# Kernel tuning notes

Hardware: AMD Instinct MI355X
Metric: run time of the kernel (lower is better)

## Reference

```python
import jax, jax.numpy as jnp
import numpy as np

EPS = 1e-4          # self.epsilon
STENCIL = 24        # fixed neighbor count


def _apply_G(x, coeffs, neighbors, N):
    """SpMV: y_i = G_ii * x_i + sum_j G_ij * x_{nbr[i,j]}.
    x: [B,N,1], coeffs: [B,N,25], neighbors: [B,N,24] (>=N means invalid)."""
    B = x.shape[0]
    mask = neighbors < N                                   # [B,N,24]
    safe = jnp.where(mask, neighbors, 0)
    x2 = x[..., 0]                                         # [B,N]
    x_nbrs = jnp.take_along_axis(x2, safe.reshape(B, -1), axis=1)
    x_nbrs = x_nbrs.reshape(B, -1, STENCIL) * mask.astype(x.dtype)
    res = x2 * coeffs[:, :, 0] + (x_nbrs * coeffs[:, :, 1:]).sum(axis=2)
    return res[..., None]                                  # [B,N,1]


def _apply_GT(x, coeffs, neighbors, N):
    """Transpose SpMV (scatter-add): y_{nbr[i,j]} += G_ij * x_i."""
    B = x.shape[0]
    mask = neighbors < N
    tgt = jnp.where(mask, neighbors, 0)                    # safe targets; masked vals are 0
    vals = (x * coeffs[:, :, 1:]) * mask.astype(x.dtype)   # [B,N,24]
    res = x[..., 0] * coeffs[:, :, 0]                      # [B,N]
    res = jax.vmap(lambda r, t, v: r.at[t].add(v))(
        res, tgt.reshape(B, -1), vals.reshape(B, -1))
    return res[..., None]                                  # [B,N,1]


def setup_inputs() -> dict:
    key = jax.random.key(0)
    kG, kAd, kAo, kw, kn = jax.random.split(key, 5)
    B, N = 2, 262144
    G_coeffs = jax.random.normal(kG, (B, N, 25), dtype=jnp.float32)
    A_diag = jax.random.normal(kAd, (B, N, 1), dtype=jnp.float32)
    A_off = jax.random.normal(kAo, (B, N, STENCIL), dtype=jnp.float32)
    w = jax.random.normal(kw, (B, N, 1), dtype=jnp.float32)
    valid_mask = jnp.ones((B, N, 1), dtype=jnp.float32)
    neighbors = jax.random.randint(kn, (B, N, STENCIL), 0, 270000, dtype=jnp.int64)
    return {"G_coeffs": G_coeffs, "A_diag": A_diag, "A_off": A_off,
            "w": w, "valid_mask": valid_mask, "neighbors": neighbors}


def reference(G_coeffs, A_diag, A_off, w, valid_mask, neighbors):
    B, N, _ = G_coeffs.shape
    active = valid_mask.sum()
    norm_A = (jnp.abs(A_diag).sum() + jnp.abs(A_off).sum()) / (active * 25 + 1e-6)
    # single probe vector (num_probe_vectors = 1)
    wm = w * valid_mask                                    # probe, masked
    u = _apply_GT(wm, G_coeffs, neighbors, N)
    v = _apply_G(u, G_coeffs, neighbors, N) + EPS * wm
    A_coeffs = jnp.concatenate([A_diag, A_off], axis=2)    # [B,N,25]
    y = _apply_G(v, A_coeffs, neighbors, N)
    z = y / (norm_A + 1e-8)
    diff = (z - wm) * valid_mask
    return (diff ** 2).sum() / (valid_mask.sum() + 1e-6)
```

## Files before the change

kernel.cpp:

```cpp
#include <hip/hip_runtime.h>
#include <stdint.h>

#define STENCIL 24
#define EPS_F 1e-4f
#define BLK 256
#define NXCD 8

#define NODE_N 262144
#define BIN_NODES 2048
#define LBINS 128
#define NBINS 256
#define BIN_CAP_G 49152

#define S_THREADS 512
#define S_EPT 8
#define EDGES_PER_BLOCK (S_THREADS * S_EPT)

typedef int   i32x2 __attribute__((ext_vector_type(2)));
typedef float f32x4 __attribute__((ext_vector_type(4)));

template <typename T>
static __device__ __forceinline__ T ntload(const T* p) {
    return __builtin_nontemporal_load(p);
}

static __device__ __forceinline__ int get_xcc_id() {
    int x;
    asm volatile("s_getreg_b32 %0, hwreg(HW_REG_XCC_ID)" : "=s"(x));
    return x & (NXCD - 1);
}

__device__ __forceinline__ float wave_reduce_f32(float v) {
    #pragma unroll
    for (int off = 32; off > 0; off >>= 1)
        v += __shfl_down(v, off, 64);
    return v;
}

__device__ __forceinline__ void block_reduce5(float v[5], float out[5]) {
    __shared__ float sw[4][5];
    #pragma unroll
    for (int c = 0; c < 5; ++c) v[c] = wave_reduce_f32(v[c]);
    if ((threadIdx.x & 63) == 0) {
        #pragma unroll
        for (int c = 0; c < 5; ++c) sw[threadIdx.x >> 6][c] = v[c];
    }
    __syncthreads();
    if (threadIdx.x == 0) {
        #pragma unroll
        for (int c = 0; c < 5; ++c)
            out[c] = sw[0][c] + sw[1][c] + sw[2][c] + sw[3][c];
    }
}

__global__ __launch_bounds__(S_THREADS)
void k_sortscatter(const float* __restrict__ G, const float* __restrict__ w,
                   const float* __restrict__ mask, const int* __restrict__ nbr,
                   float* __restrict__ u, int* __restrict__ binCnt,
                   int2* __restrict__ pairs) {
    __shared__ int2 rec[EDGES_PER_BLOCK];
    __shared__ int hist[LBINS], incl[LBINS], excl[LBINS], pos[LBINS], gb[LBINS];
    int tid = threadIdx.x;
    if (tid < LBINS) hist[tid] = 0;
    __syncthreads();

    long long blockStart = (long long)blockIdx.x * EDGES_PER_BLOCK;
    long long t0 = blockStart + (long long)tid * S_EPT;

    int nb[S_EPT];
    const int4* p4 = (const int4*)(nbr + t0);
    #pragma unroll
    for (int q = 0; q < S_EPT / 4; ++q) {
        int4 x = p4[q];
        nb[q*4] = x.x; nb[q*4+1] = x.y; nb[q*4+2] = x.z; nb[q*4+3] = x.w;
    }
    #pragma unroll
    for (int e = 0; e < S_EPT; ++e) {
        unsigned n = (unsigned)nb[e];
        if (n < (unsigned)NODE_N) atomicAdd(&hist[n >> 11], 1);
    }
    __syncthreads();

    if (tid < LBINS) incl[tid] = hist[tid];
    __syncthreads();
    for (int d = 1; d < LBINS; d <<= 1) {
        int x = 0;
        if (tid < LBINS && tid >= d) x = incl[tid - d];
        __syncthreads();
        if (tid < LBINS) incl[tid] += x;
        __syncthreads();
    }
    int batchBase = (blockStart >= (long long)NODE_N * STENCIL) ? LBINS : 0;
    if (tid < LBINS) {
        int h = hist[tid];
        int ex = incl[tid] - h;
        excl[tid] = ex;
        pos[tid]  = ex;
        gb[tid]   = h ? atomicAdd(&binCnt[batchBase + tid], h) : 0;
    }
    __syncthreads();

    long long i = t0 / STENCIL;
    int j0 = (int)(t0 - i * STENCIL);
    float wm = w[i] * mask[i];
    if (j0 == 0) u[i] = wm * G[i * 25];
    float gv[S_EPT];
    const float* grow = G + i * 25 + 1 + j0;
    #pragma unroll
    for (int e = 0; e < S_EPT; ++e) gv[e] = grow[e];
    #pragma unroll
    for (int e = 0; e < S_EPT; ++e) {
        unsigned n = (unsigned)nb[e];
        if (n < (unsigned)NODE_N) {
            int b = (int)(n >> 11);
            int lp = atomicAdd(&pos[b], 1);
            rec[lp] = make_int2((int)(n & (BIN_NODES - 1)) | (b << 11),
                                __float_as_int(wm * gv[e]));
        }
    }
    __syncthreads();

    int tot = incl[LBINS - 1];
    for (int s = tid; s < tot; s += S_THREADS) {
        int2 r = rec[s];
        int b = (r.x >> 11) & (LBINS - 1);
        int dst = gb[b] + (s - excl[b]);
        if (dst < BIN_CAP_G)
            pairs[(long long)(batchBase + b) * BIN_CAP_G + dst] =
                make_int2(r.x & (BIN_NODES - 1), r.y);
    }
}

__global__ __launch_bounds__(1024)
void k_binaccum(const int* __restrict__ binCnt, const int2* __restrict__ pairs,
                float* __restrict__ u) {
    __shared__ float acc[4][BIN_NODES + 1];
    int g = blockIdx.x, tid = threadIdx.x;
    for (int l = tid; l < BIN_NODES; l += 1024) {
        acc[0][l] = 0.f; acc[1][l] = 0.f; acc[2][l] = 0.f; acc[3][l] = 0.f;
    }
    __syncthreads();
    int cnt = binCnt[g]; if (cnt > BIN_CAP_G) cnt = BIN_CAP_G;
    const i32x2* pb = (const i32x2*)(pairs + (long long)g * BIN_CAP_G);
    int rep = tid & 3;
    for (int s = tid; s < cnt; s += 1024) {
        i32x2 r = __builtin_nontemporal_load(pb + s);
        atomicAdd(&acc[rep][r.x], __int_as_float(r.y));
    }
    __syncthreads();
    long long gbase = (long long)(g >> 7) * NODE_N + (long long)(g & (LBINS - 1)) * BIN_NODES;
    for (int l = tid; l < BIN_NODES; l += 1024)
        u[gbase + l] += acc[0][l] + acc[1][l] + acc[2][l] + acc[3][l];
}

__global__ __launch_bounds__(BLK)
void k_v(const float* __restrict__ G, const float* __restrict__ w,
         const float* __restrict__ mask, const int* __restrict__ nbr,
         const float* __restrict__ u, float* __restrict__ v, long long BN) {
    __shared__ float sg[BLK * 25];
    int tid = threadIdx.x;
    long long base = (long long)blockIdx.x * BLK;
    int rows = (int)(((BN - base) < BLK) ? (BN - base) : BLK);
    const float* gsrc = G + base * 25;
    for (int k = tid; k < rows * 25; k += BLK) sg[k] = ntload(gsrc + k);
    __syncthreads();
    if (tid >= rows) return;
    long long i = base + tid;
    const int4* nb4 = (const int4*)(nbr + i * STENCIL);
    int nn[24];
    #pragma unroll
    for (int q = 0; q < 6; ++q) {
        int4 x = nb4[q];
        nn[q*4] = x.x; nn[q*4+1] = x.y; nn[q*4+2] = x.z; nn[q*4+3] = x.w;
    }
    const float* g  = sg + tid * 25;
    const float* ub = u + (i / NODE_N) * (long long)NODE_N;
    float uv[STENCIL];
    #pragma unroll
    for (int j = 0; j < STENCIL; ++j)
        uv[j] = ub[(unsigned)nn[j] & (unsigned)(NODE_N - 1)];
    float acc = u[i] * g[0] + EPS_F * ntload(w + i) * ntload(mask + i);
    #pragma unroll
    for (int j = 0; j < STENCIL; ++j)
        acc += g[1 + j] * (((unsigned)nn[j] < (unsigned)NODE_N) ? uv[j] : 0.f);
    v[i] = acc;
}

__global__ __launch_bounds__(BLK)
void k_y2(const float* __restrict__ Ad, const float* __restrict__ Ao,
          const float* __restrict__ w, const float* __restrict__ mask,
          const int* __restrict__ nbr, const float* __restrict__ v,
          float* __restrict__ py, int nblk) {
    int tid = threadIdx.x;
    long long i0 = (long long)blockIdx.x * BLK + tid;
    long long i1 = i0 + NODE_N;
    int nn0[24], nn1[24];
    const int4* nb40 = (const int4*)(nbr + i0 * STENCIL);
    const int4* nb41 = (const int4*)(nbr + i1 * STENCIL);
    #pragma unroll
    for (int q = 0; q < 6; ++q) {
        int4 x = nb40[q];
        nn0[q*4] = x.x; nn0[q*4+1] = x.y; nn0[q*4+2] = x.z; nn0[q*4+3] = x.w;
    }
    #pragma unroll
    for (int q = 0; q < 6; ++q) {
        int4 x = nb41[q];
        nn1[q*4] = x.x; nn1[q*4+1] = x.y; nn1[q*4+2] = x.z; nn1[q*4+3] = x.w;
    }
    const float* vb0 = v;
    const float* vb1 = v + NODE_N;
    float vv0[24], vv1[24];
    unsigned valid0 = 0, valid1 = 0;
    #pragma unroll
    for (int j = 0; j < 24; ++j) {
        vv0[j] = vb0[(unsigned)nn0[j] & (unsigned)(NODE_N - 1)];
        valid0 |= ((unsigned)nn0[j] < (unsigned)NODE_N) ? (1u << j) : 0u;
    }
    #pragma unroll
    for (int j = 0; j < 24; ++j) {
        vv1[j] = vb1[(unsigned)nn1[j] & (unsigned)(NODE_N - 1)];
        valid1 |= ((unsigned)nn1[j] < (unsigned)NODE_N) ? (1u << j) : 0u;
    }
    float a0[24], a1[24];
    const f32x4* ar0 = (const f32x4*)(Ao + i0 * STENCIL);
    const f32x4* ar1 = (const f32x4*)(Ao + i1 * STENCIL);
    #pragma unroll
    for (int q = 0; q < 6; ++q) {
        f32x4 x = ntload(ar0 + q);
        a0[q*4] = x.x; a0[q*4+1] = x.y; a0[q*4+2] = x.z; a0[q*4+3] = x.w;
    }
    #pragma unroll
    for (int q = 0; q < 6; ++q) {
        f32x4 x = ntload(ar1 + q);
        a1[q*4] = x.x; a1[q*4+1] = x.y; a1[q*4+2] = x.z; a1[q*4+3] = x.w;
    }
    float ad0 = ntload(Ad + i0),  ad1 = ntload(Ad + i1);
    float m0  = ntload(mask + i0), m1 = ntload(mask + i1);
    float w0  = ntload(w + i0),    w1 = ntload(w + i1);
    float vi0 = v[i0], vi1 = v[i1];
    float asum = fabsf(ad0) + fabsf(ad1);
    #pragma unroll
    for (int j = 0; j < 24; ++j) asum += fabsf(a0[j]) + fabsf(a1[j]);
    float acc0 = vi0 * ad0, acc1 = vi1 * ad1;
    #pragma unroll
    for (int j = 0; j < 24; ++j) {
        acc0 += a0[j] * (((valid0 >> j) & 1u) ? vv0[j] : 0.f);
        acc1 += a1[j] * (((valid1 >> j) & 1u) ? vv1[j] : 0.f);
    }
    float P0 = acc0 * m0, P1 = acc1 * m1;
    float Q0 = w0 * m0 * m0, Q1 = w1 * m1 * m1;
    float part[5] = {asum, m0 + m1, P0*P0 + P1*P1, P0*Q0 + P1*Q1, Q0*Q0 + Q1*Q1};
    float out[5];
    block_reduce5(part, out);
    if (tid == 0) {
        #pragma unroll
        for (int c = 0; c < 5; ++c) py[(long long)c * nblk + blockIdx.x] = out[c];
    }
}

__global__ __launch_bounds__(BLK)
void k_y(const float* __restrict__ Ad, const float* __restrict__ Ao,
         const float* __restrict__ w, const float* __restrict__ mask,
         const int* __restrict__ nbr, const float* __restrict__ v,
         float* __restrict__ py, int nblk, long long BN) {
    int tid = threadIdx.x;
    long long base = (long long)blockIdx.x * BLK;
    int rows = (int)(((BN - base) < BLK) ? (BN - base) : BLK);
    float part[5] = {0.f, 0.f, 0.f, 0.f, 0.f};
    if (tid < rows) {
        long long i = base + tid;
        const int4* nb4 = (const int4*)(nbr + i * STENCIL);
        int nn[24];
        #pragma unroll
        for (int q = 0; q < 6; ++q) {
            int4 x = nb4[q];
            nn[q*4] = x.x; nn[q*4+1] = x.y; nn[q*4+2] = x.z; nn[q*4+3] = x.w;
        }
        const float* vb = v + (i / NODE_N) * (long long)NODE_N;
        float vv[STENCIL];
        #pragma unroll
        for (int j = 0; j < STENCIL; ++j)
            vv[j] = vb[(unsigned)nn[j] & (unsigned)(NODE_N - 1)];
        float a[STENCIL];
        const f32x4* ar = (const f32x4*)(Ao + i * STENCIL);
        #pragma unroll
        for (int q = 0; q < 6; ++q) {
            f32x4 x = ntload(ar + q);
            a[q*4] = x.x; a[q*4+1] = x.y; a[q*4+2] = x.z; a[q*4+3] = x.w;
        }
        float ad = ntload(Ad + i);
        float m  = ntload(mask + i);
        float wv = ntload(w + i);
        float asum = fabsf(ad);
        #pragma unroll
        for (int j = 0; j < STENCIL; ++j) asum += fabsf(a[j]);
        float acc = v[i] * ad;
        #pragma unroll
        for (int j = 0; j < STENCIL; ++j)
            acc += a[j] * (((unsigned)nn[j] < (unsigned)NODE_N) ? vv[j] : 0.f);
        float P = acc * m;
        float Q = wv * m * m;
        part[0] = asum;
        part[1] = m;
        part[2] = P * P;
        part[3] = P * Q;
        part[4] = Q * Q;
    }
    float out[5];
    block_reduce5(part, out);
    if (tid == 0) {
        #pragma unroll
        for (int c = 0; c < 5; ++c) py[(long long)c * nblk + blockIdx.x] = out[c];
    }
}

__global__ __launch_bounds__(1024)
void k_final(const float* __restrict__ py, int nblk, float* __restrict__ out) {
    __shared__ float sw[16][5];
    __shared__ float res[5];
    float part[5] = {0.f, 0.f, 0.f, 0.f, 0.f};
    for (int t = threadIdx.x; t < nblk; t += 1024) {
        #pragma unroll
        for (int c = 0; c < 5; ++c) part[c] += py[(long long)c * nblk + t];
    }
    #pragma unroll
    for (int c = 0; c < 5; ++c) part[c] = wave_reduce_f32(part[c]);
    if ((threadIdx.x & 63) == 0) {
        #pragma unroll
        for (int c = 0; c < 5; ++c) sw[threadIdx.x >> 6][c] = part[c];
    }
    __syncthreads();
    if (threadIdx.x == 0) {
        #pragma unroll
        for (int c = 0; c < 5; ++c) {
            float r = 0.f;
            for (int k = 0; k < 16; ++k) r += sw[k][c];
            res[c] = r;
        }
        double A   = res[0], act = res[1];
        double a   = res[2], b   = res[3], c2 = res[4];
        double nrm = A / (act * 25.0 + 1e-6) + 1e-8;
        double loss = (a / (nrm * nrm) - 2.0 * b / nrm + c2) / (act + 1e-6);
        out[0] = (float)loss;
    }
}

__global__ void k_init_fb(const float* __restrict__ G, const float* __restrict__ w,
                          const float* __restrict__ mask, float* __restrict__ u, long long BN) {
    long long i = (long long)blockIdx.x * blockDim.x + threadIdx.x;
    if (i < BN) u[i] = w[i] * mask[i] * G[i * 25];
}
__global__ void k_scatter_fb(const float* __restrict__ G, const float* __restrict__ w,
                             const float* __restrict__ mask, const int* __restrict__ nbr,
                             float* __restrict__ ucopy, int N, long long BN) {
    long long t = (long long)blockIdx.x * blockDim.x + threadIdx.x;
    if (t >= BN * STENCIL) return;
    long long i = t / STENCIL;
    int j = (int)(t - i * STENCIL);
    int n = nbr[t];
    if ((unsigned)n >= (unsigned)N) return;
    float wm = w[i] * mask[i];
    float gv = G[i * 25 + 1 + j];
    float* ub = ucopy + (long long)get_xcc_id() * BN + (i / N) * (long long)N;
    __hip_atomic_fetch_add(&ub[n], wm * gv, __ATOMIC_RELAXED, __HIP_MEMORY_SCOPE_WORKGROUP);
}
__global__ void k_usum_fb(const float* __restrict__ ucopy, float* __restrict__ u, long long BN) {
    long long i = (long long)blockIdx.x * blockDim.x + threadIdx.x;
    if (i >= BN) return;
    float acc = u[i];
    #pragma unroll
    for (int c = 0; c < NXCD; ++c) acc += ucopy[(long long)c * BN + i];
    u[i] = acc;
}

extern "C" void kernel_launch(void* const* d_in, const int* in_sizes, int n_in,
                              void* d_out, int out_size, void* d_ws, size_t ws_size,
                              hipStream_t stream) {
    const float* G    = (const float*)d_in[0];
    const float* Ad   = (const float*)d_in[1];
    const float* Ao   = (const float*)d_in[2];
    const float* w    = (const float*)d_in[3];
    const float* mask = (const float*)d_in[4];
    const int*   nbr  = (const int*)d_in[5];

    const long long BN = in_sizes[3];
    const long long nEdges = BN * STENCIL;
    const int nodeBlocks = (int)((BN + BLK - 1) / BLK);

    float* u  = (float*)d_ws;
    float* v  = u + BN;
    float* py = v + BN;
    char*  after_common = (char*)(py + 5LL * nodeBlocks);

    int*  binCnt = (int*)(((uintptr_t)after_common + 15) & ~(uintptr_t)15);
    int2* pairs  = (int2*)(((uintptr_t)(binCnt + NBINS) + 7) & ~(uintptr_t)7);
    size_t need_fast = (size_t)((char*)(pairs + (long long)NBINS * BIN_CAP_G) - (char*)d_ws);

    float* ucopy = (float*)(((uintptr_t)after_common + 15) & ~(uintptr_t)15);

    bool fast = (BN == 2LL * NODE_N) && (nEdges % EDGES_PER_BLOCK == 0) &&
                (ws_size >= need_fast);

    if (fast) {
        hipMemsetAsync(binCnt, 0, NBINS * sizeof(int), stream);
        int gridS = (int)(nEdges / EDGES_PER_BLOCK);
        k_sortscatter<<<gridS, S_THREADS, 0, stream>>>(G, w, mask, nbr, u, binCnt, pairs);
        k_binaccum<<<NBINS, 1024, 0, stream>>>(binCnt, pairs, u);
        k_v<<<nodeBlocks, BLK, 0, stream>>>(G, w, mask, nbr, u, v, BN);
        int yBlocks = NODE_N / BLK;
        k_y2<<<yBlocks, BLK, 0, stream>>>(Ad, Ao, w, mask, nbr, v, py, yBlocks);
        k_final<<<1, 1024, 0, stream>>>(py, yBlocks, (float*)d_out);
    } else {
        hipMemsetAsync(ucopy, 0, (size_t)NXCD * BN * sizeof(float), stream);
        int edgeBlocks = (int)((nEdges + BLK - 1) / BLK);
        k_init_fb<<<nodeBlocks, BLK, 0, stream>>>(G, w, mask, u, BN);
        k_scatter_fb<<<edgeBlocks, BLK, 0, stream>>>(G, w, mask, nbr, ucopy, NODE_N, BN);
        k_usum_fb<<<nodeBlocks, BLK, 0, stream>>>(ucopy, u, BN);
        k_v<<<nodeBlocks, BLK, 0, stream>>>(G, w, mask, nbr, u, v, BN);
        k_y<<<nodeBlocks, BLK, 0, stream>>>(Ad, Ao, w, mask, nbr, v, py, nodeBlocks, BN);
        k_final<<<1, 1024, 0, stream>>>(py, nodeBlocks, (float*)d_out);
    }
}
```

Before: 400.4 us.

## Replace binned pair buffer and accumulation pass with direct sorted global atomics

The transpose scatter no longer writes locally sorted (index, value) pairs to a global binned buffer for a second kernel to accumulate in shared memory. Each block now issues float atomicAdds straight into u in the bin-sorted order, and u is zeroed by a memset while the diagonal term is also added atomically. This drops one kernel launch and the write and re-read of the pairs buffer, at the cost of many global atomics whose per-block locality is only partial. It also removes the capacity clamp that silently dropped overflowing edges.

Measured after the change: 816.1 us. 104% more time.

```diff
diff --git a/kernel.cpp b/kernel.cpp
--- a/kernel.cpp
+++ b/kernel.cpp
@@ -9,8 +9,6 @@
 #define NODE_N 262144
 #define BIN_NODES 2048
 #define LBINS 128
-#define NBINS 256
-#define BIN_CAP_G 49152
 
 #define S_THREADS 512
 #define S_EPT 8
@@ -56,10 +54,9 @@
 __global__ __launch_bounds__(S_THREADS)
 void k_sortscatter(const float* __restrict__ G, const float* __restrict__ w,
                    const float* __restrict__ mask, const int* __restrict__ nbr,
-                   float* __restrict__ u, int* __restrict__ binCnt,
-                   int2* __restrict__ pairs) {
+                   float* __restrict__ u) {
     __shared__ int2 rec[EDGES_PER_BLOCK];
-    __shared__ int hist[LBINS], incl[LBINS], excl[LBINS], pos[LBINS], gb[LBINS];
+    __shared__ int hist[LBINS], incl[LBINS], pos[LBINS];
     int tid = threadIdx.x;
     if (tid < LBINS) hist[tid] = 0;
     __syncthreads();
@@ -90,20 +87,13 @@
         if (tid < LBINS) incl[tid] += x;
         __syncthreads();
     }
-    int batchBase = (blockStart >= (long long)NODE_N * STENCIL) ? LBINS : 0;
-    if (tid < LBINS) {
-        int h = hist[tid];
-        int ex = incl[tid] - h;
-        excl[tid] = ex;
-        pos[tid]  = ex;
-        gb[tid]   = h ? atomicAdd(&binCnt[batchBase + tid], h) : 0;
-    }
+    if (tid < LBINS) pos[tid] = incl[tid] - hist[tid];
     __syncthreads();
 
     long long i = t0 / STENCIL;
     int j0 = (int)(t0 - i * STENCIL);
     float wm = w[i] * mask[i];
-    if (j0 == 0) u[i] = wm * G[i * 25];
+    if (j0 == 0) atomicAdd(&u[i], wm * G[i * 25]);
     float gv[S_EPT];
     const float* grow = G + i * 25 + 1 + j0;
     #pragma unroll
@@ -120,37 +110,14 @@
     }
     __syncthreads();
 
+    long long ubase = (blockStart >= (long long)NODE_N * STENCIL) ? NODE_N : 0;
     int tot = incl[LBINS - 1];
     for (int s = tid; s < tot; s += S_THREADS) {
         int2 r = rec[s];
-        int b = (r.x >> 11) & (LBINS - 1);
-        int dst = gb[b] + (s - excl[b]);
-        if (dst < BIN_CAP_G)
-            pairs[(long long)(batchBase + b) * BIN_CAP_G + dst] =
-                make_int2(r.x & (BIN_NODES - 1), r.y);
-    }
-}
-
-__global__ __launch_bounds__(1024)
-void k_binaccum(const int* __restrict__ binCnt, const int2* __restrict__ pairs,
-                float* __restrict__ u) {
-    __shared__ float acc[4][BIN_NODES + 1];
-    int g = blockIdx.x, tid = threadIdx.x;
-    for (int l = tid; l < BIN_NODES; l += 1024) {
-        acc[0][l] = 0.f; acc[1][l] = 0.f; acc[2][l] = 0.f; acc[3][l] = 0.f;
-    }
-    __syncthreads();
-    int cnt = binCnt[g]; if (cnt > BIN_CAP_G) cnt = BIN_CAP_G;
-    const i32x2* pb = (const i32x2*)(pairs + (long long)g * BIN_CAP_G);
-    int rep = tid & 3;
-    for (int s = tid; s < cnt; s += 1024) {
-        i32x2 r = __builtin_nontemporal_load(pb + s);
-        atomicAdd(&acc[rep][r.x], __int_as_float(r.y));
-    }
-    __syncthreads();
-    long long gbase = (long long)(g >> 7) * NODE_N + (long long)(g & (LBINS - 1)) * BIN_NODES;
-    for (int l = tid; l < BIN_NODES; l += 1024)
-        u[gbase + l] += acc[0][l] + acc[1][l] + acc[2][l] + acc[3][l];
+        int b     = (r.x >> 11) & (LBINS - 1);
+        int local = r.x & (BIN_NODES - 1);
+        atomicAdd(&u[ubase + ((long long)b << 11) + local], __int_as_float(r.y));
+    }
 }
 
 __global__ __launch_bounds__(BLK)
@@ -392,20 +359,15 @@
     float* py = v + BN;
     char*  after_common = (char*)(py + 5LL * nodeBlocks);
 
-    int*  binCnt = (int*)(((uintptr_t)after_common + 15) & ~(uintptr_t)15);
-    int2* pairs  = (int2*)(((uintptr_t)(binCnt + NBINS) + 7) & ~(uintptr_t)7);
-    size_t need_fast = (size_t)((char*)(pairs + (long long)NBINS * BIN_CAP_G) - (char*)d_ws);
-
     float* ucopy = (float*)(((uintptr_t)after_common + 15) & ~(uintptr_t)15);
 
     bool fast = (BN == 2LL * NODE_N) && (nEdges % EDGES_PER_BLOCK == 0) &&
-                (ws_size >= need_fast);
+                (ws_size >= (size_t)((char*)after_common - (char*)d_ws));
 
     if (fast) {
-        hipMemsetAsync(binCnt, 0, NBINS * sizeof(int), stream);
+        hipMemsetAsync(u, 0, (size_t)BN * sizeof(float), stream);
         int gridS = (int)(nEdges / EDGES_PER_BLOCK);
-        k_sortscatter<<<gridS, S_THREADS, 0, stream>>>(G, w, mask, nbr, u, binCnt, pairs);
-        k_binaccum<<<NBINS, 1024, 0, stream>>>(binCnt, pairs, u);
+        k_sortscatter<<<gridS, S_THREADS, 0, stream>>>(G, w, mask, nbr, u);
         k_v<<<nodeBlocks, BLK, 0, stream>>>(G, w, mask, nbr, u, v, BN);
         int yBlocks = NODE_N / BLK;
         k_y2<<<yBlocks, BLK, 0, stream>>>(Ad, Ao, w, mask, nbr, v, py, yBlocks);
```
